# Optimization experiments

Measured on AMD Instinct MI355X. Metric: run time of the kernel, lower is better.

The kernel has to match this reference:

```python
import jax, jax.numpy as jnp
import numpy as np

A = 384          # number of nodes
F = 128          # dim_feature
C = 32           # dim_outerproduct
NT = 4           # num_transition -> hidden = F*NT
EPS = 1e-5       # NORM_SMALL


def layer_norm(x, scale, bias, eps=EPS):
    mu = jnp.mean(x, axis=-1, keepdims=True)
    var = jnp.mean(jnp.square(x - mu), axis=-1, keepdims=True)
    return (x - mu) * jax.lax.rsqrt(var + eps) * scale + bias


def setup_inputs() -> dict:
    key = jax.random.key(0)
    ks = jax.random.split(key, 12)
    d = {
        "node_vec": jax.random.normal(ks[0], (A, F), dtype=jnp.float32),
        "edge_vec": jax.random.normal(ks[1], (A, A, F), dtype=jnp.float32),
        "node_mask": jnp.ones((A,), dtype=jnp.float32),
        "edge_mask": jnp.ones((A, A), dtype=jnp.float32),
        # OuterProduct params
        "op_ln_scale": jnp.ones((F,), jnp.float32),
        "op_ln_bias": jnp.zeros((F,), jnp.float32),
        "w_left": jax.random.normal(ks[2], (F, C), jnp.float32) / np.sqrt(F),
        "b_left": jnp.zeros((C,), jnp.float32),
        "w_right": jax.random.normal(ks[3], (F, C), jnp.float32) / np.sqrt(F),
        "b_right": jnp.zeros((C,), jnp.float32),
        "w_out": jax.random.normal(ks[4], (C * C, F), jnp.float32) / np.sqrt(C * C),
        "b_out": jnp.zeros((F,), jnp.float32),
        # Transition params
        "tr_ln_scale": jnp.ones((F,), jnp.float32),
        "tr_ln_bias": jnp.zeros((F,), jnp.float32),
        "w_t1": jax.random.normal(ks[5], (F, F * NT), jnp.float32) / np.sqrt(F),
        "b_t1": jnp.zeros((F * NT,), jnp.float32),
        "w_t2": jax.random.normal(ks[6], (F * NT, F), jnp.float32) / np.sqrt(F * NT),
        "b_t2": jnp.zeros((F,), jnp.float32),
    }
    return d


def reference(node_vec, edge_vec, node_mask, edge_mask,
              op_ln_scale, op_ln_bias, w_left, b_left, w_right, b_right,
              w_out, b_out, tr_ln_scale, tr_ln_bias, w_t1, b_t1, w_t2, b_t2):
    # ---- OuterProduct ----
    act = layer_norm(node_vec, op_ln_scale, op_ln_bias)          # [A, F]
    left = (act @ w_left + b_left) * node_mask[:, None]          # [A, C]
    right = (act @ w_right + b_right) * node_mask[:, None]       # [A, C]
    # original: [C*A,1] @ [1,A*C] -> reshape (C,A,A,C) -> transpose (1,2,0,3)
    # which is exactly op[a,b,c,d] = left[a,c] * right[b,d]
    op = jnp.einsum('ac,bd->abcd', left, right).reshape(A, A, C * C)
    op = op @ w_out + b_out                                      # [A, A, F]
    edge = edge_vec + op
    # ---- Transition (pre-norm MLP, relu) ----
    t = layer_norm(edge, tr_ln_scale, tr_ln_bias)
    t = jax.nn.relu(t @ w_t1 + b_t1)
    t = t @ w_t2 + b_t2
    return edge + t
```

## Files before the change

kernel.cpp:

```cpp
#include <hip/hip_runtime.h>
#include <stdint.h>
#include <stddef.h>

#define A_N 384
#define F_N 128
#define C_N 32
#define H_N 512
#define LN_EPS 1e-5f

typedef unsigned short u16;
typedef _Float16 f16;
typedef f16 f16x8 __attribute__((ext_vector_type(8)));
typedef float f32x4 __attribute__((ext_vector_type(4)));

__device__ f16   gLh[A_N * C_N];
__device__ f16   gRh[A_N * C_N];
__device__ f16   gWoT[F_N * C_N * C_N];
__device__ f16   gMh[A_N * F_N * C_N];
__device__ int4  gW1P[16 * 512];
__device__ int4  gW2P[16 * 768];

__device__ __forceinline__ float b2f(u16 u) {
    union { float f; uint32_t i; } v; v.i = ((uint32_t)u) << 16; return v.f;
}
__device__ __forceinline__ float ld(const void* p, int idx, bool isbf) {
    if (isbf) return b2f(((const u16*)p)[idx]);
    return ((const float*)p)[idx];
}
__device__ __forceinline__ bool probe_bf16(const void* node_mask) {
    return ((const u16*)node_mask)[0] == 0x3F80u;
}
__device__ __forceinline__ f16x8 ldfrag(const void* p) {
    union { int4 i; f16x8 h; } u; u.i = *(const int4*)p; return u.h;
}
__device__ __forceinline__ void gload16(const void* gsrc, void* ldst) {
    __builtin_amdgcn_global_load_lds(
        (const __attribute__((address_space(1))) void*)gsrc,
        (__attribute__((address_space(3))) void*)ldst, 16, 0, 0);
}

__global__ __launch_bounds__(128) void k_pre(
    const void* __restrict__ node_vec, const void* __restrict__ node_mask,
    const void* __restrict__ op_scale, const void* __restrict__ op_bias,
    const void* __restrict__ w_left, const void* __restrict__ b_left,
    const void* __restrict__ w_right, const void* __restrict__ b_right,
    const void* __restrict__ w_out, const void* __restrict__ w_t1,
    const void* __restrict__ w_t2) {
    bool isbf = probe_bf16(node_mask);
    const int t = threadIdx.x;
    if (blockIdx.x < 384) {
        __shared__ float sAct[F_N];
        __shared__ float sRed[4];
        int a = blockIdx.x;
        int f = t;
        float x = ld(node_vec, a * F_N + f, isbf);
        float s1 = x, s2 = x * x;
        for (int o = 1; o < 64; o <<= 1) { s1 += __shfl_xor(s1, o); s2 += __shfl_xor(s2, o); }
        int wv = t >> 6;
        if ((t & 63) == 0) { sRed[wv * 2] = s1; sRed[wv * 2 + 1] = s2; }
        __syncthreads();
        float sum = sRed[0] + sRed[2], sq = sRed[1] + sRed[3];
        float mu = sum * (1.0f / F_N);
        float var = sq * (1.0f / F_N) - mu * mu;
        float rs = rsqrtf(var + LN_EPS);
        sAct[f] = (x - mu) * rs * ld(op_scale, f, isbf) + ld(op_bias, f, isbf);
        __syncthreads();
        if (t < 64) {
            int c = t & 31;
            bool isL = t < 32;
            const void* W = isL ? w_left : w_right;
            const void* B = isL ? b_left : b_right;
            float acc = ld(B, c, isbf);
            for (int ff = 0; ff < F_N; ff++) acc += sAct[ff] * ld(W, ff * C_N + c, isbf);
            acc *= ld(node_mask, a, isbf);
            if (isL) gLh[a * C_N + c] = (f16)acc;
            else     gRh[a * C_N + c] = (f16)acc;
        }
    } else if (blockIdx.x < 448) {
        int s = (blockIdx.x - 384) * 128 + t;
        int ch = s >> 9, r = s & 511, n = r >> 4, sgq = r & 15;
        int h = ch * 32 + n;
        union { int4 i; f16 hh[8]; } u;
        #pragma unroll
        for (int e = 0; e < 8; e++) u.hh[e] = (f16)ld(w_t1, (sgq * 8 + e) * H_N + h, isbf);
        gW1P[ch * 512 + n * 16 + (sgq ^ (n & 7))] = u.i;
    } else if (blockIdx.x < 512) {
        int s = (blockIdx.x - 448) * 128 + t;
        int ch = s >> 9, r = s & 511, f = r >> 2, hb = r & 3;
        union { int4 i; f16 hh[8]; } u;
        #pragma unroll
        for (int e = 0; e < 8; e++) u.hh[e] = (f16)ld(w_t2, (ch * 32 + hb * 8 + e) * F_N + f, isbf);
        gW2P[(size_t)ch * 768 + f * 5 + hb] = u.i;
    } else {
        int row = (blockIdx.x - 512) * 128 + t;
        int c = row & 31, f = row >> 5;
        union { int4 i4[4]; f16 h[32]; } u;
        #pragma unroll
        for (int d = 0; d < 32; d++) u.h[d] = (f16)ld(w_out, (c * 32 + d) * F_N + f, isbf);
        int4* dst = (int4*)(gWoT + (size_t)row * 32);
        dst[0] = u.i4[0]; dst[1] = u.i4[1]; dst[2] = u.i4[2]; dst[3] = u.i4[3];
    }
}

__global__ __launch_bounds__(256) void k_mgemm() {
    const int t = threadIdx.x;
    const int lane = t & 63, wid = t >> 6;
    const int g = lane >> 4, fc = lane & 15;
    const int bw = wid >> 1, cw = wid & 1;
    const int bg = blockIdx.x >> 4, fg = blockIdx.x & 15;
    const int b0w = bg * 32 + bw * 16;
    const int fc0 = fg * 256 + cw * 128;
    const f32x4 zero4 = (f32x4){0.f, 0.f, 0.f, 0.f};

    f16x8 afr = ldfrag(gRh + (b0w + fc) * C_N + g * 8);
    f32x4 acc[8];
    #pragma unroll
    for (int nc = 0; nc < 8; nc++) {
        f16x8 bfr = ldfrag(gWoT + (size_t)(fc0 + nc * 16 + fc) * 32 + g * 8);
        acc[nc] = __builtin_amdgcn_mfma_f32_16x16x32_f16(afr, bfr, zero4, 0, 0, 0);
    }
    #pragma unroll
    for (int nc = 0; nc < 8; nc++) {
        int col = fc0 + nc * 16 + fc;
        #pragma unroll
        for (int rg = 0; rg < 4; rg++) {
            int b = b0w + g * 4 + rg;
            gMh[(size_t)b * 4096 + col] = (f16)acc[nc][rg];
        }
    }
}

#define SM_W1   0
#define SM_W2   16384
#define SM_RED  16384
#define SM_H    40960
#define SM_B1   46080
#define SM_SCL  48128
#define SM_BIA  48640
#define SM_B2   49152
#define SM_BOUT 49664
#define SM_TOT  50176

__global__ __launch_bounds__(256, 3) void k_fused(
    const void* __restrict__ edge_vec, const void* __restrict__ b_out,
    const void* __restrict__ tr_scale, const void* __restrict__ tr_bias,
    const void* __restrict__ b_t1, const void* __restrict__ b_t2,
    const void* __restrict__ node_mask, float* __restrict__ out)
{
    bool isbf = probe_bf16(node_mask);
    __shared__ __align__(16) unsigned char smem[SM_TOT];
    float* sRed   = (float*)(smem + SM_RED);
    float* sB1    = (float*)(smem + SM_B1);
    float* sScale = (float*)(smem + SM_SCL);
    float* sBias  = (float*)(smem + SM_BIA);
    float* sB2    = (float*)(smem + SM_B2);
    float* sBout  = (float*)(smem + SM_BOUT);

    const int t = threadIdx.x;
    const int lane = t & 63, wid = t >> 6;
    const int g = lane >> 4, fc = lane & 15;
    const int wr = wid >> 1, wc = wid & 1;

    const int L = blockIdx.x;
    const int xcd = L & 7, pos = L >> 3;
    const int bx = xcd * 12 + (pos % 12);
    const int by = pos / 12;
    const int a0 = by * 16, b0 = bx * 4;

    sB1[t]       = ld(b_t1, t, isbf);
    sB1[t + 256] = ld(b_t1, t + 256, isbf);
    if (t < 128) {
        sScale[t] = ld(tr_scale, t, isbf);
        sBias[t]  = ld(tr_bias, t, isbf);
        sB2[t]    = ld(b_t2, t, isbf);
        sBout[t]  = ld(b_out, t, isbf);
    }
    __syncthreads();

    f32x4 acc2[2][4];
    const f32x4 zero4 = (f32x4){0.f, 0.f, 0.f, 0.f};
    f16x8 aL = ldfrag(gLh + (a0 + fc) * C_N + g * 8);
    #pragma unroll
    for (int bb = 0; bb < 2; bb++) {
        int b = b0 + wr * 2 + bb;
        #pragma unroll
        for (int nc = 0; nc < 4; nc++) {
            int f = wc * 64 + nc * 16 + fc;
            f16x8 bM = ldfrag(gMh + ((size_t)(b * F_N + f)) * C_N + g * 8);
            acc2[bb][nc] = __builtin_amdgcn_mfma_f32_16x16x32_f16(aL, bM, zero4, 0, 0, 0);
        }
    }
    #pragma unroll
    for (int bb = 0; bb < 2; bb++) {
        int b = b0 + wr * 2 + bb;
        #pragma unroll
        for (int nc = 0; nc < 4; nc++) {
            int f = wc * 64 + nc * 16 + fc;
            float bo = sBout[f];
            #pragma unroll
            for (int rg = 0; rg < 4; rg++) {
                int a = a0 + g * 4 + rg;
                acc2[bb][nc][rg] += ld(edge_vec, (a * A_N + b) * F_N + f, isbf) + bo;
            }
        }
    }
    float pA[2][4], qA[2][4];
    #pragma unroll
    for (int bb = 0; bb < 2; bb++)
        #pragma unroll
        for (int rg = 0; rg < 4; rg++) {
            float e0 = acc2[bb][0][rg], e1 = acc2[bb][1][rg];
            float e2 = acc2[bb][2][rg], e3 = acc2[bb][3][rg];
            float p = e0 + e1 + e2 + e3;
            float q = e0 * e0 + e1 * e1 + e2 * e2 + e3 * e3;
            p += __shfl_xor(p, 1); q += __shfl_xor(q, 1);
            p += __shfl_xor(p, 2); q += __shfl_xor(q, 2);
            p += __shfl_xor(p, 4); q += __shfl_xor(q, 4);
            p += __shfl_xor(p, 8); q += __shfl_xor(q, 8);
            pA[bb][rg] = p; qA[bb][rg] = q;
            if (fc == 0) {
                int r = wr * 32 + bb * 16 + g * 4 + rg;
                sRed[r * 4 + wc * 2]     = p;
                sRed[r * 4 + wc * 2 + 1] = q;
            }
        }
    __syncthreads();
    float muA[2][4], rsA[2][4];
    #pragma unroll
    for (int bb = 0; bb < 2; bb++)
        #pragma unroll
        for (int rg = 0; rg < 4; rg++) {
            int r = wr * 32 + bb * 16 + g * 4 + rg;
            float s1 = pA[bb][rg] + sRed[r * 4 + (wc ^ 1) * 2];
            float s2 = qA[bb][rg] + sRed[r * 4 + (wc ^ 1) * 2 + 1];
            float mu = s1 * (1.0f / F_N);
            float var = s2 * (1.0f / F_N) - mu * mu;
            muA[bb][rg] = mu;
            rsA[bb][rg] = rsqrtf(var + LN_EPS);
        }
    #pragma unroll
    for (int bb = 0; bb < 2; bb++)
        #pragma unroll
        for (int nc = 0; nc < 4; nc++) {
            int f = wc * 64 + nc * 16 + fc;
            float sc = sScale[f], bi = sBias[f];
            #pragma unroll
            for (int rg = 0; rg < 4; rg++) {
                int r = wr * 32 + bb * 16 + g * 4 + rg;
                float x = (acc2[bb][nc][rg] - muA[bb][rg]) * rsA[bb][rg] * sc + bi;
                *(f16*)(smem + r * 256 + ((f * 2) ^ ((r & 7) << 4))) = (f16)x;
            }
        }
    __syncthreads();

    f16x8 a1[2][4];
    #pragma unroll
    for (int mr = 0; mr < 2; mr++)
        #pragma unroll
        for (int ks = 0; ks < 4; ks++) {
            int r = wr * 32 + mr * 16 + fc;
            a1[mr][ks] = ldfrag(smem + r * 256 + ((ks * 64 + g * 16) ^ ((r & 7) << 4)));
        }
    __syncthreads();

    {
        #pragma unroll
        for (int i = 0; i < 2; i++) {
            int s = i * 4 + wid;
            gload16(gW1P + 0 * 512 + s * 64 + lane, smem + SM_W1 + 0 * 8192 + s * 1024);
        }
        #pragma unroll
        for (int i = 0; i < 3; i++) {
            int s = i * 4 + wid;
            gload16(gW2P + (size_t)0 * 768 + s * 64 + lane, smem + SM_W2 + 0 * 12288 + s * 1024);
        }
    }
    __syncthreads();

    for (int ch = 0; ch < 16; ch++) {
        const int cur = ch & 1;
        const int h0 = ch * 32;

        if (ch < 15) {
            const int nxt = cur ^ 1;
            #pragma unroll
            for (int i = 0; i < 2; i++) {
                int s = i * 4 + wid;
                gload16(gW1P + (ch + 1) * 512 + s * 64 + lane,
                        smem + SM_W1 + nxt * 8192 + s * 1024);
            }
            #pragma unroll
            for (int i = 0; i < 3; i++) {
                int s = i * 4 + wid;
                gload16(gW2P + (size_t)(ch + 1) * 768 + s * 64 + lane,
                        smem + SM_W2 + nxt * 12288 + s * 1024);
            }
        }

        f32x4 acc1[2];
        acc1[0] = zero4; acc1[1] = zero4;
        __builtin_amdgcn_s_setprio(1);
        #pragma unroll
        for (int ks = 0; ks < 4; ks++) {
            int n = wc * 16 + fc;
            f16x8 bfr = ldfrag(smem + SM_W1 + cur * 8192 + n * 256 +
                               ((ks * 64 + g * 16) ^ ((n & 7) << 4)));
            #pragma unroll
            for (int mr = 0; mr < 2; mr++)
                acc1[mr] = __builtin_amdgcn_mfma_f32_16x16x32_f16(a1[mr][ks], bfr, acc1[mr], 0, 0, 0);
        }
        __builtin_amdgcn_s_setprio(0);
        {
            int jl = wc * 16 + fc;
            float b1v = sB1[h0 + jl];
            #pragma unroll
            for (int mr = 0; mr < 2; mr++)
                #pragma unroll
                for (int rg = 0; rg < 4; rg++) {
                    int r2 = wr * 32 + mr * 16 + g * 4 + rg;
                    *(f16*)(smem + SM_H + r2 * 80 + jl * 2) =
                        (f16)fmaxf(acc1[mr][rg] + b1v, 0.f);
                }
        }
        __syncthreads();

        __builtin_amdgcn_s_setprio(1);
        {
            f16x8 afr2[2], bfr2[4];
            #pragma unroll
            for (int mr = 0; mr < 2; mr++) {
                int r = wr * 32 + mr * 16 + fc;
                afr2[mr] = ldfrag(smem + SM_H + r * 80 + g * 16);
            }
            #pragma unroll
            for (int nc = 0; nc < 4; nc++) {
                int fR = wc * 64 + nc * 16 + fc;
                bfr2[nc] = ldfrag(smem + SM_W2 + cur * 12288 + fR * 80 + g * 16);
            }
            #pragma unroll
            for (int mr = 0; mr < 2; mr++)
                #pragma unroll
                for (int nc = 0; nc < 4; nc++)
                    acc2[mr][nc] = __builtin_amdgcn_mfma_f32_16x16x32_f16(
                        afr2[mr], bfr2[nc], acc2[mr][nc], 0, 0, 0);
        }
        __builtin_amdgcn_s_setprio(0);
        __syncthreads();
    }

    #pragma unroll
    for (int bb = 0; bb < 2; bb++) {
        int b = b0 + wr * 2 + bb;
        #pragma unroll
        for (int nc = 0; nc < 4; nc++) {
            int f = wc * 64 + nc * 16 + fc;
            float b2v = sB2[f];
            #pragma unroll
            for (int rg = 0; rg < 4; rg++) {
                int a = a0 + g * 4 + rg;
                out[((size_t)a * A_N + b) * F_N + f] = acc2[bb][nc][rg] + b2v;
            }
        }
    }
}

extern "C" void kernel_launch(void* const* d_in, const int* in_sizes, int n_in,
                              void* d_out, int out_size, void* d_ws, size_t ws_size,
                              hipStream_t stream) {
    const void* node_vec  = d_in[0];
    const void* edge_vec  = d_in[1];
    const void* node_mask = d_in[2];
    const void* op_scale  = d_in[4];
    const void* op_bias   = d_in[5];
    const void* w_left    = d_in[6];
    const void* b_left    = d_in[7];
    const void* w_right   = d_in[8];
    const void* b_right   = d_in[9];
    const void* w_out     = d_in[10];
    const void* b_out     = d_in[11];
    const void* tr_scale  = d_in[12];
    const void* tr_bias   = d_in[13];
    const void* w_t1      = d_in[14];
    const void* b_t1      = d_in[15];
    const void* w_t2      = d_in[16];
    const void* b_t2      = d_in[17];
    float* out = (float*)d_out;
    (void)d_ws; (void)ws_size; (void)in_sizes; (void)n_in; (void)out_size;

    hipLaunchKernelGGL(k_pre, dim3(544), dim3(128), 0, stream,
                       node_vec, node_mask, op_scale, op_bias,
                       w_left, b_left, w_right, b_right, w_out, w_t1, w_t2);
    hipLaunchKernelGGL(k_mgemm, dim3(192), dim3(256), 0, stream);
    hipLaunchKernelGGL(k_fused, dim3(2304), dim3(256), 0, stream,
                       edge_vec, b_out, tr_scale, tr_bias, b_t1, b_t2, node_mask, out);
}
```

Before: 250.3 us.

## Give each wave a full 16-row tile to drop cross-wave reductions and barriers

Each wave now owns one b column with all 128 features (16 rows) instead of splitting rows and features across a 2x2 wave grid. LayerNorm statistics are reduced entirely within the wave by shuffles, which removes the shared-memory reduction buffer and two block barriers. In the transition loop each wave reads back only its own hidden rows, so the barrier between the first and second GEMM is removed. The cost is that every wave now loads the full W1 and W2 fragments from LDS (more LDS reads per MFMA) and holds 8 accumulator tiles.

Result: no change. 253.4 us (+1.2%).

```diff
diff --git a/kernel.cpp b/kernel.cpp
--- a/kernel.cpp
+++ b/kernel.cpp
@@ -132,7 +132,6 @@
 
 #define SM_W1   0
 #define SM_W2   16384
-#define SM_RED  16384
 #define SM_H    40960
 #define SM_B1   46080
 #define SM_SCL  48128
@@ -149,7 +148,6 @@
 {
     bool isbf = probe_bf16(node_mask);
     __shared__ __align__(16) unsigned char smem[SM_TOT];
-    float* sRed   = (float*)(smem + SM_RED);
     float* sB1    = (float*)(smem + SM_B1);
     float* sScale = (float*)(smem + SM_SCL);
     float* sBias  = (float*)(smem + SM_BIA);
@@ -159,13 +157,13 @@
     const int t = threadIdx.x;
     const int lane = t & 63, wid = t >> 6;
     const int g = lane >> 4, fc = lane & 15;
-    const int wr = wid >> 1, wc = wid & 1;
 
     const int L = blockIdx.x;
     const int xcd = L & 7, pos = L >> 3;
     const int bx = xcd * 12 + (pos % 12);
     const int by = pos / 12;
     const int a0 = by * 16, b0 = bx * 4;
+    const int b = b0 + wid;
 
     sB1[t]       = ld(b_t1, t, isbf);
     sB1[t + 256] = ld(b_t1, t + 256, isbf);
@@ -177,103 +175,67 @@
     }
     __syncthreads();
 
-    f32x4 acc2[2][4];
     const f32x4 zero4 = (f32x4){0.f, 0.f, 0.f, 0.f};
+    f32x4 acc2[8];
     f16x8 aL = ldfrag(gLh + (a0 + fc) * C_N + g * 8);
     #pragma unroll
-    for (int bb = 0; bb < 2; bb++) {
-        int b = b0 + wr * 2 + bb;
-        #pragma unroll
-        for (int nc = 0; nc < 4; nc++) {
-            int f = wc * 64 + nc * 16 + fc;
-            f16x8 bM = ldfrag(gMh + ((size_t)(b * F_N + f)) * C_N + g * 8);
-            acc2[bb][nc] = __builtin_amdgcn_mfma_f32_16x16x32_f16(aL, bM, zero4, 0, 0, 0);
-        }
-    }
-    #pragma unroll
-    for (int bb = 0; bb < 2; bb++) {
-        int b = b0 + wr * 2 + bb;
-        #pragma unroll
-        for (int nc = 0; nc < 4; nc++) {
-            int f = wc * 64 + nc * 16 + fc;
-            float bo = sBout[f];
-            #pragma unroll
-            for (int rg = 0; rg < 4; rg++) {
-                int a = a0 + g * 4 + rg;
-                acc2[bb][nc][rg] += ld(edge_vec, (a * A_N + b) * F_N + f, isbf) + bo;
-            }
-        }
-    }
-    float pA[2][4], qA[2][4];
-    #pragma unroll
-    for (int bb = 0; bb < 2; bb++)
+    for (int nc = 0; nc < 8; nc++) {
+        int f = nc * 16 + fc;
+        f16x8 bM = ldfrag(gMh + ((size_t)(b * F_N + f)) * C_N + g * 8);
+        acc2[nc] = __builtin_amdgcn_mfma_f32_16x16x32_f16(aL, bM, zero4, 0, 0, 0);
+    }
+    #pragma unroll
+    for (int nc = 0; nc < 8; nc++) {
+        int f = nc * 16 + fc;
+        float bo = sBout[f];
         #pragma unroll
         for (int rg = 0; rg < 4; rg++) {
-            float e0 = acc2[bb][0][rg], e1 = acc2[bb][1][rg];
-            float e2 = acc2[bb][2][rg], e3 = acc2[bb][3][rg];
-            float p = e0 + e1 + e2 + e3;
-            float q = e0 * e0 + e1 * e1 + e2 * e2 + e3 * e3;
-            p += __shfl_xor(p, 1); q += __shfl_xor(q, 1);
-            p += __shfl_xor(p, 2); q += __shfl_xor(q, 2);
-            p += __shfl_xor(p, 4); q += __shfl_xor(q, 4);
-            p += __shfl_xor(p, 8); q += __shfl_xor(q, 8);
-            pA[bb][rg] = p; qA[bb][rg] = q;
-            if (fc == 0) {
-                int r = wr * 32 + bb * 16 + g * 4 + rg;
-                sRed[r * 4 + wc * 2]     = p;
-                sRed[r * 4 + wc * 2 + 1] = q;
-            }
-        }
+            int a = a0 + g * 4 + rg;
+            acc2[nc][rg] += ld(edge_vec, (a * A_N + b) * F_N + f, isbf) + bo;
+        }
+    }
+    float mu[4], rs[4];
+    #pragma unroll
+    for (int rg = 0; rg < 4; rg++) {
+        float p = 0.f, q = 0.f;
+        #pragma unroll
+        for (int nc = 0; nc < 8; nc++) { float e = acc2[nc][rg]; p += e; q += e * e; }
+        p += __shfl_xor(p, 1); q += __shfl_xor(q, 1);
+        p += __shfl_xor(p, 2); q += __shfl_xor(q, 2);
+        p += __shfl_xor(p, 4); q += __shfl_xor(q, 4);
+        p += __shfl_xor(p, 8); q += __shfl_xor(q, 8);
+        float m = p * (1.0f / F_N);
+        mu[rg] = m;
+        rs[rg] = rsqrtf(q * (1.0f / F_N) - m * m + LN_EPS);
+    }
+    #pragma unroll
+    for (int nc = 0; nc < 8; nc++) {
+        int f = nc * 16 + fc;
+        float sc = sScale[f], bi = sBias[f];
+        #pragma unroll
+        for (int rg = 0; rg < 4; rg++) {
+            int r = wid * 16 + g * 4 + rg;
+            float x = (acc2[nc][rg] - mu[rg]) * rs[rg] * sc + bi;
+            *(f16*)(smem + r * 256 + ((f * 2) ^ ((r & 7) << 4))) = (f16)x;
+        }
+    }
+    f16x8 a1[4];
+    #pragma unroll
+    for (int ks = 0; ks < 4; ks++) {
+        int r = wid * 16 + fc;
+        a1[ks] = ldfrag(smem + r * 256 + ((ks * 64 + g * 16) ^ ((r & 7) << 4)));
+    }
     __syncthreads();
-    float muA[2][4], rsA[2][4];
-    #pragma unroll
-    for (int bb = 0; bb < 2; bb++)
-        #pragma unroll
-        for (int rg = 0; rg < 4; rg++) {
-            int r = wr * 32 + bb * 16 + g * 4 + rg;
-            float s1 = pA[bb][rg] + sRed[r * 4 + (wc ^ 1) * 2];
-            float s2 = qA[bb][rg] + sRed[r * 4 + (wc ^ 1) * 2 + 1];
-            float mu = s1 * (1.0f / F_N);
-            float var = s2 * (1.0f / F_N) - mu * mu;
-            muA[bb][rg] = mu;
-            rsA[bb][rg] = rsqrtf(var + LN_EPS);
-        }
-    #pragma unroll
-    for (int bb = 0; bb < 2; bb++)
-        #pragma unroll
-        for (int nc = 0; nc < 4; nc++) {
-            int f = wc * 64 + nc * 16 + fc;
-            float sc = sScale[f], bi = sBias[f];
-            #pragma unroll
-            for (int rg = 0; rg < 4; rg++) {
-                int r = wr * 32 + bb * 16 + g * 4 + rg;
-                float x = (acc2[bb][nc][rg] - muA[bb][rg]) * rsA[bb][rg] * sc + bi;
-                *(f16*)(smem + r * 256 + ((f * 2) ^ ((r & 7) << 4))) = (f16)x;
-            }
-        }
-    __syncthreads();
-
-    f16x8 a1[2][4];
-    #pragma unroll
-    for (int mr = 0; mr < 2; mr++)
-        #pragma unroll
-        for (int ks = 0; ks < 4; ks++) {
-            int r = wr * 32 + mr * 16 + fc;
-            a1[mr][ks] = ldfrag(smem + r * 256 + ((ks * 64 + g * 16) ^ ((r & 7) << 4)));
-        }
-    __syncthreads();
-
-    {
-        #pragma unroll
-        for (int i = 0; i < 2; i++) {
-            int s = i * 4 + wid;
-            gload16(gW1P + 0 * 512 + s * 64 + lane, smem + SM_W1 + 0 * 8192 + s * 1024);
-        }
-        #pragma unroll
-        for (int i = 0; i < 3; i++) {
-            int s = i * 4 + wid;
-            gload16(gW2P + (size_t)0 * 768 + s * 64 + lane, smem + SM_W2 + 0 * 12288 + s * 1024);
-        }
+
+    #pragma unroll
+    for (int i = 0; i < 2; i++) {
+        int s = i * 4 + wid;
+        gload16(gW1P + s * 64 + lane, smem + SM_W1 + s * 1024);
+    }
+    #pragma unroll
+    for (int i = 0; i < 3; i++) {
+        int s = i * 4 + wid;
+        gload16(gW2P + s * 64 + lane, smem + SM_W2 + s * 1024);
     }
     __syncthreads();
 
@@ -302,64 +264,45 @@
         __builtin_amdgcn_s_setprio(1);
         #pragma unroll
         for (int ks = 0; ks < 4; ks++) {
-            int n = wc * 16 + fc;
-            f16x8 bfr = ldfrag(smem + SM_W1 + cur * 8192 + n * 256 +
-                               ((ks * 64 + g * 16) ^ ((n & 7) << 4)));
             #pragma unroll
-            for (int mr = 0; mr < 2; mr++)
-                acc1[mr] = __builtin_amdgcn_mfma_f32_16x16x32_f16(a1[mr][ks], bfr, acc1[mr], 0, 0, 0);
+            for (int nt = 0; nt < 2; nt++) {
+                int n = nt * 16 + fc;
+                f16x8 bfr = ldfrag(smem + SM_W1 + cur * 8192 + n * 256 +
+                                   ((ks * 64 + g * 16) ^ ((n & 7) << 4)));
+                acc1[nt] = __builtin_amdgcn_mfma_f32_16x16x32_f16(a1[ks], bfr, acc1[nt], 0, 0, 0);
+            }
         }
         __builtin_amdgcn_s_setprio(0);
-        {
-            int jl = wc * 16 + fc;
-            float b1v = sB1[h0 + jl];
+        #pragma unroll
+        for (int nt = 0; nt < 2; nt++) {
+            int h = nt * 16 + fc;
+            float b1v = sB1[h0 + h];
             #pragma unroll
-            for (int mr = 0; mr < 2; mr++)
-                #pragma unroll
-                for (int rg = 0; rg < 4; rg++) {
-                    int r2 = wr * 32 + mr * 16 + g * 4 + rg;
-                    *(f16*)(smem + SM_H + r2 * 80 + jl * 2) =
-                        (f16)fmaxf(acc1[mr][rg] + b1v, 0.f);
-                }
-        }
-        __syncthreads();
-
+            for (int rg = 0; rg < 4; rg++) {
+                int r2 = wid * 16 + g * 4 + rg;
+                *(f16*)(smem + SM_H + r2 * 80 + h * 2) = (f16)fmaxf(acc1[nt][rg] + b1v, 0.f);
+            }
+        }
         __builtin_amdgcn_s_setprio(1);
-        {
-            f16x8 afr2[2], bfr2[4];
-            #pragma unroll
-            for (int mr = 0; mr < 2; mr++) {
-                int r = wr * 32 + mr * 16 + fc;
-                afr2[mr] = ldfrag(smem + SM_H + r * 80 + g * 16);
-            }
-            #pragma unroll
-            for (int nc = 0; nc < 4; nc++) {
-                int fR = wc * 64 + nc * 16 + fc;
-                bfr2[nc] = ldfrag(smem + SM_W2 + cur * 12288 + fR * 80 + g * 16);
-            }
-            #pragma unroll
-            for (int mr = 0; mr < 2; mr++)
-                #pragma unroll
-                for (int nc = 0; nc < 4; nc++)
-                    acc2[mr][nc] = __builtin_amdgcn_mfma_f32_16x16x32_f16(
-                        afr2[mr], bfr2[nc], acc2[mr][nc], 0, 0, 0);
+        f16x8 afr2 = ldfrag(smem + SM_H + (wid * 16 + fc) * 80 + g * 16);
+        #pragma unroll
+        for (int nc = 0; nc < 8; nc++) {
+            int f = nc * 16 + fc;
+            f16x8 bfr2 = ldfrag(smem + SM_W2 + cur * 12288 + f * 80 + g * 16);
+            acc2[nc] = __builtin_amdgcn_mfma_f32_16x16x32_f16(afr2, bfr2, acc2[nc], 0, 0, 0);
         }
         __builtin_amdgcn_s_setprio(0);
         __syncthreads();
     }
 
     #pragma unroll
-    for (int bb = 0; bb < 2; bb++) {
-        int b = b0 + wr * 2 + bb;
-        #pragma unroll
-        for (int nc = 0; nc < 4; nc++) {
-            int f = wc * 64 + nc * 16 + fc;
-            float b2v = sB2[f];
-            #pragma unroll
-            for (int rg = 0; rg < 4; rg++) {
-                int a = a0 + g * 4 + rg;
-                out[((size_t)a * A_N + b) * F_N + f] = acc2[bb][nc][rg] + b2v;
-            }
+    for (int nc = 0; nc < 8; nc++) {
+        int f = nc * 16 + fc;
+        float b2v = sB2[f];
+        #pragma unroll
+        for (int rg = 0; rg < 4; rg++) {
+            int a = a0 + g * 4 + rg;
+            out[((size_t)a * A_N + b) * F_N + f] = acc2[nc][rg] + b2v;
         }
     }
 }
```

## Load W2 fragments directly from global into registers, double-buffer H, drop sync

Applied to the files above, without the earlier changes.

W2 weights are now stored in a contiguous fragment-friendly layout and read straight from global (L2) into registers each chunk, instead of being staged through LDS with async copies. This frees the LDS region that held W2, shrinking shared memory so four blocks per CU can be resident, and the hidden-activation buffer is double-buffered so the trailing barrier per chunk can be removed. The trade-off is more global/L2 traffic per wave and exposed global-load latency inside the loop, plus reliance on the double-buffered H and W1 buffers to keep the single remaining barrier per chunk sufficient for correctness.

Result: no change. 246.4 us (-1.6%).

```diff
diff --git a/kernel.cpp b/kernel.cpp
--- a/kernel.cpp
+++ b/kernel.cpp
@@ -18,7 +18,7 @@
 __device__ f16   gWoT[F_N * C_N * C_N];
 __device__ f16   gMh[A_N * F_N * C_N];
 __device__ int4  gW1P[16 * 512];
-__device__ int4  gW2P[16 * 768];
+__device__ f16   gW2C[16 * F_N * 32];
 
 __device__ __forceinline__ float b2f(u16 u) {
     union { float f; uint32_t i; } v; v.i = ((uint32_t)u) << 16; return v.f;
@@ -32,6 +32,9 @@
 }
 __device__ __forceinline__ f16x8 ldfrag(const void* p) {
     union { int4 i; f16x8 h; } u; u.i = *(const int4*)p; return u.h;
+}
+__device__ __forceinline__ f16x8 asfrag(int4 v) {
+    union { int4 i; f16x8 h; } u; u.i = v; return u.h;
 }
 __device__ __forceinline__ void gload16(const void* gsrc, void* ldst) {
     __builtin_amdgcn_global_load_lds(
@@ -90,7 +93,7 @@
         union { int4 i; f16 hh[8]; } u;
         #pragma unroll
         for (int e = 0; e < 8; e++) u.hh[e] = (f16)ld(w_t2, (ch * 32 + hb * 8 + e) * F_N + f, isbf);
-        gW2P[(size_t)ch * 768 + f * 5 + hb] = u.i;
+        *(int4*)(gW2C + (size_t)ch * 4096 + f * 32 + hb * 8) = u.i;
     } else {
         int row = (blockIdx.x - 512) * 128 + t;
         int c = row & 31, f = row >> 5;
@@ -131,17 +134,16 @@
 }
 
 #define SM_W1   0
-#define SM_W2   16384
-#define SM_RED  16384
-#define SM_H    40960
-#define SM_B1   46080
-#define SM_SCL  48128
-#define SM_BIA  48640
-#define SM_B2   49152
-#define SM_BOUT 49664
-#define SM_TOT  50176
-
-__global__ __launch_bounds__(256, 3) void k_fused(
+#define SM_H    16384
+#define SM_RED  26624
+#define SM_B1   27648
+#define SM_SCL  29696
+#define SM_BIA  30208
+#define SM_B2   30720
+#define SM_BOUT 31232
+#define SM_TOT  31744
+
+__global__ __launch_bounds__(256, 4) void k_fused(
     const void* __restrict__ edge_vec, const void* __restrict__ b_out,
     const void* __restrict__ tr_scale, const void* __restrict__ tr_bias,
     const void* __restrict__ b_t1, const void* __restrict__ b_t2,
@@ -263,37 +265,30 @@
         }
     __syncthreads();
 
-    {
-        #pragma unroll
-        for (int i = 0; i < 2; i++) {
-            int s = i * 4 + wid;
-            gload16(gW1P + 0 * 512 + s * 64 + lane, smem + SM_W1 + 0 * 8192 + s * 1024);
-        }
-        #pragma unroll
-        for (int i = 0; i < 3; i++) {
-            int s = i * 4 + wid;
-            gload16(gW2P + (size_t)0 * 768 + s * 64 + lane, smem + SM_W2 + 0 * 12288 + s * 1024);
-        }
-    }
-    __syncthreads();
-
+    #pragma unroll
+    for (int i = 0; i < 2; i++) {
+        int s = i * 4 + wid;
+        gload16(gW1P + s * 64 + lane, smem + SM_W1 + s * 1024);
+    }
+    __syncthreads();
+
+    const f16* w2base = gW2C + (wc * 64 + fc) * 32 + g * 8;
     for (int ch = 0; ch < 16; ch++) {
         const int cur = ch & 1;
         const int h0 = ch * 32;
 
+        const f16* wb = w2base + (size_t)ch * 4096;
+        int4 w2ra = *(const int4*)(wb);
+        int4 w2rb = *(const int4*)(wb + 512);
+        int4 w2rc = *(const int4*)(wb + 1024);
+        int4 w2rd = *(const int4*)(wb + 1536);
+
         if (ch < 15) {
-            const int nxt = cur ^ 1;
             #pragma unroll
             for (int i = 0; i < 2; i++) {
                 int s = i * 4 + wid;
                 gload16(gW1P + (ch + 1) * 512 + s * 64 + lane,
-                        smem + SM_W1 + nxt * 8192 + s * 1024);
-            }
-            #pragma unroll
-            for (int i = 0; i < 3; i++) {
-                int s = i * 4 + wid;
-                gload16(gW2P + (size_t)(ch + 1) * 768 + s * 64 + lane,
-                        smem + SM_W2 + nxt * 12288 + s * 1024);
+                        smem + SM_W1 + (cur ^ 1) * 8192 + s * 1024);
             }
         }
 
@@ -318,7 +313,7 @@
                 #pragma unroll
                 for (int rg = 0; rg < 4; rg++) {
                     int r2 = wr * 32 + mr * 16 + g * 4 + rg;
-                    *(f16*)(smem + SM_H + r2 * 80 + jl * 2) =
+                    *(f16*)(smem + SM_H + cur * 5120 + r2 * 80 + jl * 2) =
                         (f16)fmaxf(acc1[mr][rg] + b1v, 0.f);
                 }
         }
@@ -326,26 +321,19 @@
 
         __builtin_amdgcn_s_setprio(1);
         {
-            f16x8 afr2[2], bfr2[4];
-            #pragma unroll
-            for (int mr = 0; mr < 2; mr++) {
-                int r = wr * 32 + mr * 16 + fc;
-                afr2[mr] = ldfrag(smem + SM_H + r * 80 + g * 16);
-            }
-            #pragma unroll
-            for (int nc = 0; nc < 4; nc++) {
-                int fR = wc * 64 + nc * 16 + fc;
-                bfr2[nc] = ldfrag(smem + SM_W2 + cur * 12288 + fR * 80 + g * 16);
-            }
-            #pragma unroll
-            for (int mr = 0; mr < 2; mr++)
-                #pragma unroll
-                for (int nc = 0; nc < 4; nc++)
-                    acc2[mr][nc] = __builtin_amdgcn_mfma_f32_16x16x32_f16(
-                        afr2[mr], bfr2[nc], acc2[mr][nc], 0, 0, 0);
+            f16x8 afr0 = ldfrag(smem + SM_H + cur * 5120 + (wr * 32 + fc) * 80 + g * 16);
+            f16x8 afr1 = ldfrag(smem + SM_H + cur * 5120 + (wr * 32 + 16 + fc) * 80 + g * 16);
+            f16x8 b0f = asfrag(w2ra), b1f = asfrag(w2rb), b2f2 = asfrag(w2rc), b3f = asfrag(w2rd);
+            acc2[0][0] = __builtin_amdgcn_mfma_f32_16x16x32_f16(afr0, b0f, acc2[0][0], 0, 0, 0);
+            acc2[1][0] = __builtin_amdgcn_mfma_f32_16x16x32_f16(afr1, b0f, acc2[1][0], 0, 0, 0);
+            acc2[0][1] = __builtin_amdgcn_mfma_f32_16x16x32_f16(afr0, b1f, acc2[0][1], 0, 0, 0);
+            acc2[1][1] = __builtin_amdgcn_mfma_f32_16x16x32_f16(afr1, b1f, acc2[1][1], 0, 0, 0);
+            acc2[0][2] = __builtin_amdgcn_mfma_f32_16x16x32_f16(afr0, b2f2, acc2[0][2], 0, 0, 0);
+            acc2[1][2] = __builtin_amdgcn_mfma_f32_16x16x32_f16(afr1, b2f2, acc2[1][2], 0, 0, 0);
+            acc2[0][3] = __builtin_amdgcn_mfma_f32_16x16x32_f16(afr0, b3f, acc2[0][3], 0, 0, 0);
+            acc2[1][3] = __builtin_amdgcn_mfma_f32_16x16x32_f16(afr1, b3f, acc2[1][3], 0, 0, 0);
         }
         __builtin_amdgcn_s_setprio(0);
-        __syncthreads();
     }
 
     #pragma unroll
```
